# Performance work log

Hardware: AMD Instinct MI355X
Metric: run time of the kernel (lower is better)

## Reference

```python
import jax, jax.numpy as jnp
import numpy as np

DIM = 1024
NUM_HEAD = 16
DIM_HEAD = DIM // NUM_HEAD
MAX_SEQ_LEN = 4096
RMS_EPS = 1.1920928955078125e-07  # torch nn.RMSNorm default eps = finfo(fp32).eps
LIN_EPS = 1e-6
PAD_VAL = 1.0
THETA = 10000.0


def rmsnorm(x, g):
    return x * jax.lax.rsqrt(jnp.mean(x * x, axis=-1, keepdims=True) + RMS_EPS) * g


def setup_inputs() -> dict:
    key = jax.random.key(0)
    ks = jax.random.split(key, 20)
    B, L, C, D = 4, 2048, 256, DIM
    s = 1.0 / np.sqrt(D)
    inp = {
        "x": jax.random.normal(ks[0], (B, L, D), jnp.float32),
        "context": jax.random.normal(ks[1], (B, C, D), jnp.float32),
        "attn_mask": jax.random.randint(ks[2], (B, L, L), 0, 2).astype(bool),
        "start_pos": jax.random.randint(ks[3], (B,), 0, MAX_SEQ_LEN - L).astype(jnp.int64),
        "Wqkv": jax.random.normal(ks[4], (D, 3 * D), jnp.float32) * s,
        "bqkv": jax.random.normal(ks[5], (3 * D,), jnp.float32) * 0.01,
        "g_q": jnp.ones((D,), jnp.float32),
        "g_k": jnp.ones((D,), jnp.float32),
        "cWqkv": jax.random.normal(ks[6], (D, 3 * D), jnp.float32) * s,
        "cbqkv": jax.random.normal(ks[7], (3 * D,), jnp.float32) * 0.01,
        "cg_q": jnp.ones((D,), jnp.float32),
        "cg_k": jnp.ones((D,), jnp.float32),
        "Wout": jax.random.normal(ks[8], (D, D), jnp.float32) * s,
        "bout": jax.random.normal(ks[9], (D,), jnp.float32) * 0.01,
        "g_out": jnp.ones((D,), jnp.float32),
        "cWout": jax.random.normal(ks[10], (D, D), jnp.float32) * s,
        "cbout": jax.random.normal(ks[11], (D,), jnp.float32) * 0.01,
        "cg_out": jnp.ones((D,), jnp.float32),
    }
    return inp


def _freqs(pos_indices):
    # pos_indices: (B, L) int
    inv = 1.0 / (THETA ** (jnp.arange(0, DIM_HEAD, 2, dtype=jnp.float32) / DIM_HEAD))  # (DH/2,)
    ang = pos_indices.astype(jnp.float32)[..., None] * inv  # (B, L, DH/2)
    return jnp.cos(ang), jnp.sin(ang)


def _apply_rope(t, cos, sin):
    # t: (B, H, L, DH); cos/sin: (B, L, DH/2) -> broadcast over head
    B, H, L, DH = t.shape
    tr = t.reshape(B, H, L, DH // 2, 2)
    t0, t1 = tr[..., 0], tr[..., 1]
    c = cos[:, None]  # (B,1,L,DH/2)
    s = sin[:, None]
    out = jnp.stack([t0 * c - t1 * s, t0 * s + t1 * c], axis=-1)
    return out.reshape(B, H, L, DH)


def _split_heads(t):
    B, L, D = t.shape
    return t.reshape(B, L, NUM_HEAD, DIM_HEAD).transpose(0, 2, 1, 3)


def _augment_mask(m, C):
    # m: (B, L, L) bool -> (B, L+C, L+C) bool
    B, L, _ = m.shape
    c_to_seq = jnp.broadcast_to(jnp.any(m, axis=1, keepdims=True), (B, C, L))
    seq_to_c = jnp.broadcast_to(jnp.any(m, axis=2, keepdims=True), (B, L, C))
    c_to_c = jnp.ones((B, C, C), bool)
    top = jnp.concatenate([m, seq_to_c], axis=2)
    bot = jnp.concatenate([c_to_seq, c_to_c], axis=2)
    return jnp.concatenate([top, bot], axis=1)


def reference(x, context, attn_mask, start_pos, Wqkv, bqkv, g_q, g_k,
              cWqkv, cbqkv, cg_q, cg_k, Wout, bout, g_out, cWout, cbout, cg_out):
    B, L, D = x.shape
    C = context.shape[1]

    q, k, v = jnp.split(x @ Wqkv + bqkv, 3, axis=-1)
    q = rmsnorm(q, g_q)
    k = rmsnorm(k, g_k)
    q, k, v = _split_heads(q), _split_heads(k), _split_heads(v)  # (B,H,L,DH)

    pos = start_pos[:, None] + jnp.arange(L, dtype=start_pos.dtype)[None]  # (B,L)
    cos, sin = _freqs(pos)
    q = _apply_rope(q, cos, sin)
    k = _apply_rope(k, cos, sin)

    cq, ck, cv = jnp.split(context @ cWqkv + cbqkv, 3, axis=-1)
    cq = rmsnorm(cq, cg_q)
    ck = rmsnorm(ck, cg_k)
    cq, ck, cv = _split_heads(cq), _split_heads(ck), _split_heads(cv)

    q = jnp.concatenate([q, cq], axis=2)  # (B,H,S,DH), S=L+C
    k = jnp.concatenate([k, ck], axis=2)
    v = jnp.concatenate([v, cv], axis=2)

    full_mask = _augment_mask(attn_mask, C)[:, None]  # (B,1,S,S)

    # linear attention: ReLU feature map + padded-value trick
    qf = jax.nn.relu(q)
    kf = jax.nn.relu(k)
    k_mask = full_mask[:, :, 0, :][..., None].astype(kf.dtype)  # (B,1,S,1)
    kf = kf * k_mask
    vpad = jnp.pad(v, ((0, 0), (0, 0), (0, 0), (0, 1)), constant_values=PAD_VAL)  # (B,H,S,DH+1)
    vk = jnp.einsum('bhse,bhsd->bhed', vpad, kf)        # (B,H,DH+1,DH)
    res = jnp.einsum('bhed,bhqd->bhqe', vk, qf)          # (B,H,S,DH+1)
    attn = res[..., :-1] / (res[..., -1:] + LIN_EPS)     # (B,H,S,DH)

    attn = attn.transpose(0, 2, 1, 3).reshape(B, L + C, D)
    x_out = rmsnorm(attn[:, :L] @ Wout + bout, g_out)
    c_out = rmsnorm(attn[:, L:] @ cWout + cbout, cg_out)
    return x_out, c_out
```

## Files before the change

### kernel.cpp

```cpp
#include <hip/hip_runtime.h>

typedef __bf16 bf16;
typedef __bf16 bf16x4 __attribute__((ext_vector_type(4)));
typedef __bf16 bf16x8 __attribute__((ext_vector_type(8)));
typedef float  floatx4 __attribute__((ext_vector_type(4)));

#define L_SEQ   2048
#define C_SEQ   256
#define S_SEQ   2304
#define NBATCH  4
#define NHEAD   16
#define DHEAD   64
#define DMODEL  1024
#define RMS_EPS 1.1920928955078125e-07f
#define LIN_EPS 1e-6f

__device__ __forceinline__ void gload_lds16(const void* g, void* l) {
  __builtin_amdgcn_global_load_lds(
      (const __attribute__((address_space(1))) void*)g,
      (__attribute__((address_space(3))) void*)l, 16, 0, 0);
}

__device__ __forceinline__ void transpose_job(
    const float* __restrict__ src, bf16* __restrict__ dst,
    int R, int C, int tb, bf16 (*tile)[33]) {
  int tilesx = C >> 5;
  int c0 = (tb % tilesx) * 32, r0 = (tb / tilesx) * 32;
  int tx = threadIdx.x & 31, ty = threadIdx.x >> 5;
  for (int i = ty; i < 32; i += 8)
    tile[i][tx] = (bf16)src[(size_t)(r0 + i) * C + c0 + tx];
  __syncthreads();
  for (int i = ty; i < 32; i += 8)
    dst[(size_t)(c0 + i) * R + r0 + tx] = tile[tx][i];
}

__device__ __forceinline__ void convert_job(
    const float* __restrict__ src, bf16* __restrict__ dst, int tb) {
  size_t i = ((size_t)tb * 256 + threadIdx.x) * 8;
  floatx4 a = *(const floatx4*)(src + i);
  floatx4 b = *(const floatx4*)(src + i + 4);
  bf16x8 o;
#pragma unroll
  for (int j = 0; j < 4; j++) { o[j] = (bf16)a[j]; o[4 + j] = (bf16)b[j]; }
  *(bf16x8*)(dst + i) = o;
}

__global__ __launch_bounds__(256) void prep(
    const float* __restrict__ Wqkv, const float* __restrict__ cWqkv,
    const float* __restrict__ Wout, const float* __restrict__ cWout,
    const float* __restrict__ x, const float* __restrict__ ctx,
    const int* __restrict__ mask, const int* __restrict__ spos,
    bf16* __restrict__ WqkvT, bf16* __restrict__ cWqkvT,
    bf16* __restrict__ WoutT, bf16* __restrict__ cWoutT,
    bf16* __restrict__ xbf, bf16* __restrict__ cbf,
    float* __restrict__ vkw, float* __restrict__ rope,
    int* __restrict__ anym) {
  __shared__ bf16 tile[32][33];
  __shared__ int sh;
  int b = blockIdx.x;
  if (b < 3072) { transpose_job(Wqkv, WqkvT, 1024, 3072, b, tile); return; }
  b -= 3072;
  if (b < 3072) { transpose_job(cWqkv, cWqkvT, 1024, 3072, b, tile); return; }
  b -= 3072;
  if (b < 1024) { transpose_job(Wout, WoutT, 1024, 1024, b, tile); return; }
  b -= 1024;
  if (b < 1024) { transpose_job(cWout, cWoutT, 1024, 1024, b, tile); return; }
  b -= 1024;
  if (b < 4096) { convert_job(x, xbf, b); return; }
  b -= 4096;
  if (b < 512) { convert_job(ctx, cbf, b); return; }
  b -= 512;
  if (b < 260) {
    int i = b * 1024 + threadIdx.x * 4;
    *(floatx4*)(vkw + i) = floatx4{0.f, 0.f, 0.f, 0.f};
    return;
  }
  b -= 260;
  if (b < 2048) {
    int t = threadIdx.x;
    int tok = b * 4 + (t >> 6);
    int bb = tok >> 11, s = tok & 2047;
    int j = t & 63, fi = j >> 1;
    float ang = (float)(spos[bb] + s) * expf((float)fi * -0.28782313662425572f);
    rope[(size_t)tok * 64 + j] = (j & 1) ? sinf(ang) : cosf(ang);
    return;
  }
  b -= 2048;
  int a = 0;
  size_t base = (size_t)b * L_SEQ * L_SEQ;
  for (int j = threadIdx.x; j < L_SEQ; j += 256) a |= mask[base + j];
  if (threadIdx.x == 0) sh = 0;
  __syncthreads();
  if (a) atomicOr(&sh, 1);
  __syncthreads();
  if (threadIdx.x == 0) anym[b] = sh;
}

template <bool SCATTER>
__global__ __launch_bounds__(256) void gemm_bias(
    const bf16* __restrict__ A1, const bf16* __restrict__ A2,
    const bf16* __restrict__ B1t, const bf16* __restrict__ B2t,
    const float* __restrict__ bias1, const float* __restrict__ bias2,
    bf16* __restrict__ C1, bf16* __restrict__ C2,
    bf16* __restrict__ qs, bf16* __restrict__ ks, bf16* __restrict__ vs,
    int N, int K, int ybound,
    int rpb1, int soff1, int rpb2, int soff2) {
  __shared__ bf16 As[2][4096];
  __shared__ bf16 Bs[2][4096];

  int nwg = gridDim.x * gridDim.y;
  int wg = blockIdx.y * gridDim.x + blockIdx.x;
  int cpx = nwg >> 3;
  wg = (wg & 7) * cpx + (wg >> 3);
  int bx = wg % gridDim.x, by = wg / gridDim.x;
  int n0 = bx * 128;
  const bf16 *Ap, *Bt;
  const float* bias;
  bf16* Cp;
  int m0, rpb, soff;
  if (by < ybound) {
    Ap = A1; Bt = B1t; bias = bias1; Cp = C1;
    m0 = by * 128; rpb = rpb1; soff = soff1;
  } else {
    Ap = A2; Bt = B2t; bias = bias2; Cp = C2;
    m0 = (by - ybound) * 128; rpb = rpb2; soff = soff2;
  }

  int t = threadIdx.x, lane = t & 63, w = t >> 6;
  int wm = (w & 1) * 64, wn = (w >> 1) * 64;
  int l16 = lane & 15, l4 = lane >> 4;

  int crow = w * 32 + (lane >> 2);
  int scol = ((((lane & 3) - ((lane >> 3) & 3)) & 3)) << 3;
  const bf16* Ab = Ap + (size_t)(m0 + crow) * K + scol;
  const bf16* Bb = Bt + (size_t)(n0 + crow) * K + scol;

  auto stage = [&](int buf, int kb) {
#pragma unroll
    for (int j = 0; j < 2; j++) {
      gload_lds16(Ab + (size_t)(j * 16) * K + kb, (char*)As[buf] + (w * 2 + j) * 1024);
      gload_lds16(Bb + (size_t)(j * 16) * K + kb, (char*)Bs[buf] + (w * 2 + j) * 1024);
    }
  };

  int co = ((l4 + ((l16 >> 1) & 3)) & 3) << 3;
  int rba = (wm + l16) * 32 + co;
  int rbb = (wn + l16) * 32 + co;

  floatx4 acc[4][4] = {};
  stage(0, 0);
  __syncthreads();
  int NTt = K >> 5;
  for (int tt = 0; tt < NTt; ++tt) {
    int p = tt & 1;
    if (tt + 1 < NTt) stage(p ^ 1, (tt + 1) << 5);
    bf16x8 bfr[4];
#pragma unroll
    for (int nt = 0; nt < 4; nt++) bfr[nt] = *(const bf16x8*)&Bs[p][rbb + nt * 512];
    __builtin_amdgcn_s_setprio(1);
#pragma unroll
    for (int mt = 0; mt < 4; mt++) {
      bf16x8 a = *(const bf16x8*)&As[p][rba + mt * 512];
#pragma unroll
      for (int nt = 0; nt < 4; nt++)
        acc[mt][nt] = __builtin_amdgcn_mfma_f32_16x16x32_bf16(a, bfr[nt], acc[mt][nt], 0, 0, 0);
    }
    __builtin_amdgcn_s_setprio(0);
    __syncthreads();
  }

#pragma unroll
  for (int mt = 0; mt < 4; mt++)
#pragma unroll
    for (int nt = 0; nt < 4; nt++) {
      int col = n0 + wn + nt * 16 + l16;
      float bval = bias[col];
      if constexpr (SCATTER) {
        int which = col >> 10;
        int h = (col >> 6) & 15;
        int dh = col & 63;
        int rmask = (1 << rpb) - 1;
        if (which == 2) {
          int rw0 = m0 + wm + mt * 16 + l4 * 4;
          int b = rw0 >> rpb;
          int s = soff + (rw0 & rmask);
          bf16x4 o;
#pragma unroll
          for (int r = 0; r < 4; r++) o[r] = (bf16)(acc[mt][nt][r] + bval);
          *(bf16x4*)(vs + ((size_t)(b * NHEAD + h) * DHEAD + dh) * S_SEQ + s) = o;
        } else {
          bf16* dst = which == 0 ? qs : ks;
#pragma unroll
          for (int r = 0; r < 4; r++) {
            int rw = m0 + wm + mt * 16 + l4 * 4 + r;
            int b = rw >> rpb;
            int s = soff + (rw & rmask);
            dst[((size_t)(b * NHEAD + h) * S_SEQ + s) * DHEAD + dh] =
                (bf16)(acc[mt][nt][r] + bval);
          }
        }
      } else {
#pragma unroll
        for (int r = 0; r < 4; r++) {
          int rw = m0 + wm + mt * 16 + l4 * 4 + r;
          Cp[(size_t)rw * N + col] = (bf16)(acc[mt][nt][r] + bval);
        }
      }
    }
}

__global__ __launch_bounds__(256) void qkv_post(
    bf16* __restrict__ qs, bf16* __restrict__ ks,
    const int* __restrict__ mask, const float* __restrict__ rope,
    const int* __restrict__ anym,
    const float* __restrict__ g_q, const float* __restrict__ g_k,
    const float* __restrict__ cg_q, const float* __restrict__ cg_k) {
  int g = blockIdx.x, t = threadIdx.x;
  bool is_ctx = g >= NBATCH * L_SEQ;
  int b, s;
  const float *gq, *gk;
  float mval;
  if (!is_ctx) {
    b = g >> 11;
    int l = g & 2047;
    s = l;
    mval = mask[(size_t)b * L_SEQ * L_SEQ + l] ? 1.f : 0.f;
    gq = g_q; gk = g_k;
  } else {
    int gg = g - NBATCH * L_SEQ;
    b = gg >> 8;
    s = L_SEQ + (gg & 255);
    mval = anym[b] ? 1.f : 0.f;
    gq = cg_q; gk = cg_k;
  }
  int d0 = t * 4;
  int h = t >> 4, dh = (t & 15) * 4;
  size_t base = ((size_t)(b * NHEAD + h) * S_SEQ + s) * DHEAD + dh;
  bf16x4 q4 = *(const bf16x4*)(qs + base);
  bf16x4 k4 = *(const bf16x4*)(ks + base);
  float qv[4], kv[4], pq = 0.f, pk = 0.f;
#pragma unroll
  for (int i = 0; i < 4; i++) {
    qv[i] = (float)q4[i]; kv[i] = (float)k4[i];
    pq += qv[i] * qv[i];  pk += kv[i] * kv[i];
  }
  int lane = t & 63, w = t >> 6;
  for (int off = 32; off > 0; off >>= 1) {
    pq += __shfl_down(pq, off, 64);
    pk += __shfl_down(pk, off, 64);
  }
  __shared__ float red[8];
  if (lane == 0) { red[w] = pq; red[4 + w] = pk; }
  __syncthreads();
  float sq = red[0] + red[1] + red[2] + red[3];
  float sk = red[4] + red[5] + red[6] + red[7];
  float scq = rsqrtf(sq * (1.f / DMODEL) + RMS_EPS);
  float sck = rsqrtf(sk * (1.f / DMODEL) + RMS_EPS);
#pragma unroll
  for (int i = 0; i < 4; i++) {
    qv[i] *= scq * gq[d0 + i];
    kv[i] *= sck * gk[d0 + i];
  }
  if (!is_ctx) {
    floatx4 tb4 = *(const floatx4*)&rope[((size_t)(b << 11 | s)) * 64 + dh];
#pragma unroll
    for (int pr = 0; pr < 2; pr++) {
      float cc = tb4[2 * pr], ss = tb4[2 * pr + 1];
      float t0 = qv[2 * pr], t1 = qv[2 * pr + 1];
      qv[2 * pr]     = t0 * cc - t1 * ss;
      qv[2 * pr + 1] = t0 * ss + t1 * cc;
      t0 = kv[2 * pr]; t1 = kv[2 * pr + 1];
      kv[2 * pr]     = t0 * cc - t1 * ss;
      kv[2 * pr + 1] = t0 * ss + t1 * cc;
    }
  }
  bf16x4 qo, ko;
#pragma unroll
  for (int i = 0; i < 4; i++) {
    qo[i] = (bf16)fmaxf(qv[i], 0.f);
    ko[i] = (bf16)(fmaxf(kv[i], 0.f) * mval);
  }
  *(bf16x4*)(qs + base) = qo;
  *(bf16x4*)(ks + base) = ko;
}

#define VK_CH   12
#define VK_SPAN (S_SEQ / VK_CH)
__global__ __launch_bounds__(256) void vk_mfma(
    const bf16* __restrict__ vT, const bf16* __restrict__ kf,
    float* __restrict__ vk) {
  __shared__ bf16 Vs[2][64][40];
  __shared__ bf16 Ks[2][64][40];
  int bh = blockIdx.x / VK_CH, chunk = blockIdx.x % VK_CH;
  int t = threadIdx.x, lane = t & 63, w = t >> 6;
  int l16 = lane & 15, l4 = lane >> 4;
  const bf16* vp = vT + (size_t)bh * DHEAD * S_SEQ;
  const bf16* kp = kf + (size_t)bh * S_SEQ * DHEAD;
  int s_begin = chunk * VK_SPAN;
  int ve = t >> 2, vso = (t & 3) * 8;
  int ks_s = t & 31, kd0 = (t >> 5) * 8;
  floatx4 acc[4] = {};
  float dsum[8] = {};
  bf16x8 vv = *(const bf16x8*)(vp + (size_t)ve * S_SEQ + s_begin + vso);
  bf16x8 kv = *(const bf16x8*)(kp + (size_t)(s_begin + ks_s) * DHEAD + kd0);
  for (int st = 0; st < VK_SPAN; st += 32) {
    int cur = (st >> 5) & 1;
    *(bf16x8*)&Vs[cur][ve][vso] = vv;
#pragma unroll
    for (int j = 0; j < 8; j++) {
      Ks[cur][kd0 + j][ks_s] = kv[j];
      dsum[j] += (float)kv[j];
    }
    if (st + 32 < VK_SPAN) {
      int s0 = s_begin + st + 32;
      vv = *(const bf16x8*)(vp + (size_t)ve * S_SEQ + s0 + vso);
      kv = *(const bf16x8*)(kp + (size_t)(s0 + ks_s) * DHEAD + kd0);
    }
    __syncthreads();
    bf16x8 af = *(const bf16x8*)&Vs[cur][w * 16 + l16][l4 * 8];
#pragma unroll
    for (int nt = 0; nt < 4; nt++) {
      bf16x8 bfr = *(const bf16x8*)&Ks[cur][nt * 16 + l16][l4 * 8];
      acc[nt] = __builtin_amdgcn_mfma_f32_16x16x32_bf16(af, bfr, acc[nt], 0, 0, 0);
    }
  }
  float* vkbh = vk + (size_t)bh * 65 * 64;
#pragma unroll
  for (int nt = 0; nt < 4; nt++)
#pragma unroll
    for (int r = 0; r < 4; r++)
      atomicAdd(&vkbh[(w * 16 + l4 * 4 + r) * 64 + nt * 16 + l16], acc[nt][r]);
#pragma unroll
  for (int j = 0; j < 8; j++)
#pragma unroll
    for (int off = 16; off > 0; off >>= 1)
      dsum[j] += __shfl_down(dsum[j], off, 32);
  if ((lane & 31) == 0)
#pragma unroll
    for (int j = 0; j < 8; j++)
      atomicAdd(&vkbh[64 * 64 + kd0 + j], dsum[j]);
}

__global__ __launch_bounds__(256) void res_attn(
    const bf16* __restrict__ qf, const float* __restrict__ vk,
    bf16* __restrict__ attn_x, bf16* __restrict__ attn_c) {
  __shared__ bf16 Bs[80][72];
  __shared__ float sden[256];
  int bh = blockIdx.x / 9, mblk = blockIdx.x % 9;
  int b = bh >> 4, h = bh & 15;
  int t = threadIdx.x, lane = t & 63, w = t >> 6;
  const float* vkp = vk + (size_t)bh * 65 * 64;
  for (int i = t; i < 80 * 64; i += 256) {
    int e = i >> 6, d = i & 63;
    Bs[e][d] = (bf16)(e < 65 ? vkp[i] : 0.f);
  }
  __syncthreads();
  int l16 = lane & 15, l4 = lane >> 4;
  const bf16* qbase = qf + (size_t)bh * S_SEQ * DHEAD;
  int q0w = mblk * 256 + w * 64;

  floatx4 acc[4][5] = {};
  bf16x8 af[4][2], bfr[5][2];
#pragma unroll
  for (int mt = 0; mt < 4; mt++) {
    int q = q0w + mt * 16 + l16;
    af[mt][0] = *(const bf16x8*)(qbase + (size_t)q * 64 + l4 * 8);
    af[mt][1] = *(const bf16x8*)(qbase + (size_t)q * 64 + 32 + l4 * 8);
  }
#pragma unroll
  for (int nt = 0; nt < 5; nt++) {
    bfr[nt][0] = *(const bf16x8*)&Bs[nt * 16 + l16][l4 * 8];
    bfr[nt][1] = *(const bf16x8*)&Bs[nt * 16 + l16][32 + l4 * 8];
  }
#pragma unroll
  for (int mt = 0; mt < 4; mt++)
#pragma unroll
    for (int nt = 0; nt < 5; nt++) {
      acc[mt][nt] = __builtin_amdgcn_mfma_f32_16x16x32_bf16(af[mt][0], bfr[nt][0], acc[mt][nt], 0, 0, 0);
      acc[mt][nt] = __builtin_amdgcn_mfma_f32_16x16x32_bf16(af[mt][1], bfr[nt][1], acc[mt][nt], 0, 0, 0);
    }
  if (l16 == 0) {
#pragma unroll
    for (int mt = 0; mt < 4; mt++)
#pragma unroll
      for (int r = 0; r < 4; r++)
        sden[w * 64 + mt * 16 + l4 * 4 + r] = acc[mt][4][r];
  }
  __syncthreads();
#pragma unroll
  for (int mt = 0; mt < 4; mt++)
#pragma unroll
    for (int r = 0; r < 4; r++) {
      float den = sden[w * 64 + mt * 16 + l4 * 4 + r] + LIN_EPS;
      float rden = 1.f / den;
      int q = q0w + mt * 16 + l4 * 4 + r;
#pragma unroll
      for (int nt = 0; nt < 4; nt++) {
        int dcol = nt * 16 + l16;
        float a = acc[mt][nt][r] * rden;
        if (q < L_SEQ)
          attn_x[((size_t)b * L_SEQ + q) * DMODEL + h * DHEAD + dcol] = (bf16)a;
        else
          attn_c[((size_t)b * C_SEQ + (q - L_SEQ)) * DMODEL + h * DHEAD + dcol] = (bf16)a;
      }
    }
}

__global__ __launch_bounds__(256) void final_norm(
    const bf16* __restrict__ y_x, const bf16* __restrict__ y_c,
    const float* __restrict__ g_out, const float* __restrict__ cg_out,
    float* __restrict__ out) {
  int g = blockIdx.x, t = threadIdx.x;
  const bf16* src;
  const float* gv;
  if (g < NBATCH * L_SEQ) {
    src = y_x + (size_t)g * DMODEL; gv = g_out;
  } else {
    int gg = g - NBATCH * L_SEQ;
    src = y_c + (size_t)gg * DMODEL; gv = cg_out;
  }
  float* dst = out + (size_t)g * DMODEL;
  int d0 = t * 4;
  bf16x4 y4 = *(const bf16x4*)(src + d0);
  float yv[4], p = 0.f;
#pragma unroll
  for (int i = 0; i < 4; i++) { yv[i] = (float)y4[i]; p += yv[i] * yv[i]; }
  int lane = t & 63, w = t >> 6;
  for (int off = 32; off > 0; off >>= 1) p += __shfl_down(p, off, 64);
  __shared__ float red[4];
  if (lane == 0) red[w] = p;
  __syncthreads();
  float ssum = red[0] + red[1] + red[2] + red[3];
  float sc = rsqrtf(ssum * (1.f / DMODEL) + RMS_EPS);
  floatx4 o;
#pragma unroll
  for (int i = 0; i < 4; i++) o[i] = yv[i] * sc * gv[d0 + i];
  *(floatx4*)(dst + d0) = o;
}

extern "C" void kernel_launch(void* const* d_in, const int* in_sizes, int n_in,
                              void* d_out, int out_size, void* d_ws, size_t ws_size,
                              hipStream_t stream) {
  const float* x      = (const float*)d_in[0];
  const float* ctx    = (const float*)d_in[1];
  const int*   mask   = (const int*)d_in[2];
  const int*   spos   = (const int*)d_in[3];
  const float* Wqkv   = (const float*)d_in[4];
  const float* bqkv   = (const float*)d_in[5];
  const float* g_q    = (const float*)d_in[6];
  const float* g_k    = (const float*)d_in[7];
  const float* cWqkv  = (const float*)d_in[8];
  const float* cbqkv  = (const float*)d_in[9];
  const float* cg_q   = (const float*)d_in[10];
  const float* cg_k   = (const float*)d_in[11];
  const float* Wout   = (const float*)d_in[12];
  const float* bout   = (const float*)d_in[13];
  const float* g_out  = (const float*)d_in[14];
  const float* cWout  = (const float*)d_in[15];
  const float* cbout  = (const float*)d_in[16];
  const float* cg_out = (const float*)d_in[17];

  char* wsp = (char*)d_ws;
  size_t off = 0;
  auto alloc = [&](size_t bytes) -> void* {
    void* p = wsp + off;
    off += (bytes + 255) & ~(size_t)255;
    return p;
  };
  bf16* WqkvT  = (bf16*)alloc((size_t)3072 * 1024 * 2);
  bf16* cWqkvT = (bf16*)alloc((size_t)3072 * 1024 * 2);
  bf16* WoutT  = (bf16*)alloc((size_t)1024 * 1024 * 2);
  bf16* cWoutT = (bf16*)alloc((size_t)1024 * 1024 * 2);
  bf16* xbf    = (bf16*)alloc((size_t)NBATCH * L_SEQ * DMODEL * 2);
  bf16* cbf    = (bf16*)alloc((size_t)NBATCH * C_SEQ * DMODEL * 2);
  const size_t SLAB = (size_t)NBATCH * NHEAD * S_SEQ * DHEAD;
  bf16* qfs    = (bf16*)alloc(SLAB * 2);
  bf16* kfs    = (bf16*)alloc(SLAB * 2);
  bf16* vfs    = (bf16*)alloc(SLAB * 2);
  float* vkw   = (float*)alloc((size_t)64 * 65 * 64 * 4);
  float* rope  = (float*)alloc((size_t)NBATCH * L_SEQ * 64 * 4);
  int* anym    = (int*)alloc(256);
  bf16* attn_x = kfs;
  bf16* attn_c = kfs + (size_t)NBATCH * L_SEQ * DMODEL;
  bf16* y_x    = vfs;
  bf16* y_c    = vfs + (size_t)NBATCH * L_SEQ * DMODEL;

  prep<<<15112, 256, 0, stream>>>(Wqkv, cWqkv, Wout, cWout, x, ctx, mask, spos,
                                  WqkvT, cWqkvT, WoutT, cWoutT, xbf, cbf,
                                  vkw, rope, anym);

  gemm_bias<true><<<dim3(24, 72), 256, 0, stream>>>(
      xbf, cbf, WqkvT, cWqkvT, bqkv, cbqkv, nullptr, nullptr,
      qfs, kfs, vfs, 3072, 1024, 64, 11, 0, 8, L_SEQ);

  qkv_post<<<NBATCH * (L_SEQ + C_SEQ), 256, 0, stream>>>(
      qfs, kfs, mask, rope, anym, g_q, g_k, cg_q, cg_k);

  vk_mfma<<<64 * VK_CH, 256, 0, stream>>>(vfs, kfs, vkw);

  res_attn<<<576, 256, 0, stream>>>(qfs, vkw, attn_x, attn_c);

  gemm_bias<false><<<dim3(8, 72), 256, 0, stream>>>(
      attn_x, attn_c, WoutT, cWoutT, bout, cbout, y_x, y_c,
      nullptr, nullptr, nullptr, 1024, 1024, 64, 0, 0, 0, 0);

  final_norm<<<NBATCH * (L_SEQ + C_SEQ), 256, 0, stream>>>(
      y_x, y_c, g_out, cg_out, (float*)d_out);
}
```

Before: 360.2 us.

## Add 256x256-tile 8-wave QKV GEMM with interleaved staged loads

Replaces the 128x128-tile QKV projection GEMM with a new kernel using 256x256 tiles, 512 threads (8 waves) and a 64-wide K step. Global-to-LDS loads are split into quarter stages spread across the MFMA phases, using a two-deep prefetch with explicit vmcnt waits and an XOR-swizzled LDS layout. The goal is more operand reuse per tile and better overlap of loads with matrix math. In exchange it uses 128 KB of LDS per block and many more accumulator registers, and the grid shrinks to 432 blocks, which may limit occupancy.

```diff
diff --git a/kernel.cpp b/kernel.cpp
--- a/kernel.cpp
+++ b/kernel.cpp
@@ -96,6 +96,142 @@
   if (threadIdx.x == 0) anym[b] = sh;
 }
 
+__global__ __launch_bounds__(512, 2) void gemm_qkv8(
+    const bf16* __restrict__ A1, const bf16* __restrict__ A2,
+    const bf16* __restrict__ B1t, const bf16* __restrict__ B2t,
+    const float* __restrict__ bias1, const float* __restrict__ bias2,
+    bf16* __restrict__ qs, bf16* __restrict__ ks, bf16* __restrict__ vs,
+    int K, int ybound, int rpb1, int soff1, int rpb2, int soff2) {
+  __shared__ bf16 As[2][256 * 64];
+  __shared__ bf16 Bs[2][256 * 64];
+
+  int nwg = gridDim.x * gridDim.y;
+  int wg = blockIdx.y * gridDim.x + blockIdx.x;
+  int cpx = nwg >> 3;
+  wg = (wg & 7) * cpx + (wg >> 3);
+  int bx = wg % gridDim.x, by = wg / gridDim.x;
+  int n0 = bx * 256;
+  const bf16 *Ap, *Bt;
+  const float* bias;
+  int m0, rpb, soff;
+  if (by < ybound) {
+    Ap = A1; Bt = B1t; bias = bias1; m0 = by * 256; rpb = rpb1; soff = soff1;
+  } else {
+    Ap = A2; Bt = B2t; bias = bias2; m0 = (by - ybound) * 256; rpb = rpb2; soff = soff2;
+  }
+
+  int t = threadIdx.x, lane = t & 63, w = t >> 6;
+  int wr = w >> 2, wc = w & 3;
+  int l16 = lane & 15, l4 = lane >> 4;
+
+  int lr = lane >> 3;
+  int lcol = ((lane & 7) ^ lr) << 3;
+  const bf16* Ag = Ap + (size_t)(m0 + lr) * K + lcol;
+  const bf16* Bg = Bt + (size_t)(n0 + lr) * K + lcol;
+
+  int cB0 = w * 2;
+  int cB1 = 16 + w * 2;
+  int cAX = ((w & 4) << 2) + (w & 3) * 2;
+  int cAY = 8 + cAX;
+
+  auto stg = [&](const bf16* G, bf16* Ldst, int c0, int kb) {
+#pragma unroll
+    for (int j = 0; j < 2; j++) {
+      int c = c0 + j;
+      gload_lds16(G + (size_t)(c * 8) * K + kb, (char*)Ldst + c * 1024);
+    }
+  };
+  auto ldf = [&](const bf16* S, int row, int ks) {
+    return *(const bf16x8*)&S[row * 64 + ((((ks << 2) + l4) ^ (l16 & 7)) << 3)];
+  };
+
+  floatx4 acc[8][4] = {};
+  int NT = K >> 6;
+  stg(Bg, Bs[0], cB0, 0);  stg(Bg, Bs[0], cB1, 0);
+  stg(Ag, As[0], cAX, 0);  stg(Ag, As[0], cAY, 0);
+  if (NT > 1) {
+    stg(Bg, Bs[1], cB0, 64); stg(Bg, Bs[1], cB1, 64);
+    stg(Ag, As[1], cAX, 64);
+  }
+  asm volatile("s_waitcnt vmcnt(6)" ::: "memory");
+  __builtin_amdgcn_s_barrier();
+
+  int pb = 0;
+  bf16x8 bfr[4][2];
+  for (int tt = 0; tt < NT; ++tt) {
+    int kb = tt << 6;
+    const bf16* Asp = As[pb];
+    const bf16* Bsp = Bs[pb];
+#pragma unroll
+    for (int p = 0; p < 4; ++p) {
+      if (p == 0) {
+#pragma unroll
+        for (int nt = 0; nt < 4; nt++) {
+          bfr[nt][0] = ldf(Bsp, wc * 64 + nt * 16 + l16, 0);
+          bfr[nt][1] = ldf(Bsp, wc * 64 + nt * 16 + l16, 1);
+        }
+      }
+      int ar = wr * 128 + p * 32 + l16;
+      bf16x8 a00 = ldf(Asp, ar, 0);
+      bf16x8 a01 = ldf(Asp, ar, 1);
+      bf16x8 a10 = ldf(Asp, ar + 16, 0);
+      bf16x8 a11 = ldf(Asp, ar + 16, 1);
+      if (p == 0)      { if (tt + 1 < NT) stg(Ag, As[pb ^ 1], cAY, kb + 64); }
+      else if (p == 1) { if (tt + 2 < NT) stg(Bg, Bs[pb], cB0, kb + 128); }
+      else if (p == 2) { if (tt + 2 < NT) stg(Bg, Bs[pb], cB1, kb + 128); }
+      else             { if (tt + 2 < NT) stg(Ag, As[pb], cAX, kb + 128); }
+      __builtin_amdgcn_s_barrier();
+      __builtin_amdgcn_s_setprio(1);
+      int mt = p * 2;
+#pragma unroll
+      for (int nt = 0; nt < 4; nt++) {
+        acc[mt][nt]     = __builtin_amdgcn_mfma_f32_16x16x32_bf16(a00, bfr[nt][0], acc[mt][nt], 0, 0, 0);
+        acc[mt][nt]     = __builtin_amdgcn_mfma_f32_16x16x32_bf16(a01, bfr[nt][1], acc[mt][nt], 0, 0, 0);
+        acc[mt + 1][nt] = __builtin_amdgcn_mfma_f32_16x16x32_bf16(a10, bfr[nt][0], acc[mt + 1][nt], 0, 0, 0);
+        acc[mt + 1][nt] = __builtin_amdgcn_mfma_f32_16x16x32_bf16(a11, bfr[nt][1], acc[mt + 1][nt], 0, 0, 0);
+      }
+      __builtin_amdgcn_s_setprio(0);
+      if (p == 3) {
+        if (tt + 2 < NT) asm volatile("s_waitcnt vmcnt(6)" ::: "memory");
+        else             asm volatile("s_waitcnt vmcnt(0)" ::: "memory");
+      }
+      __builtin_amdgcn_s_barrier();
+    }
+    pb ^= 1;
+  }
+
+#pragma unroll
+  for (int mt = 0; mt < 8; mt++)
+#pragma unroll
+    for (int nt = 0; nt < 4; nt++) {
+      int col = n0 + wc * 64 + nt * 16 + l16;
+      float bval = bias[col];
+      int which = col >> 10;
+      int h = (col >> 6) & 15;
+      int dh = col & 63;
+      int rmask = (1 << rpb) - 1;
+      if (which == 2) {
+        int rw0 = m0 + wr * 128 + mt * 16 + l4 * 4;
+        int b = rw0 >> rpb;
+        int s = soff + (rw0 & rmask);
+        bf16x4 o;
+#pragma unroll
+        for (int r = 0; r < 4; r++) o[r] = (bf16)(acc[mt][nt][r] + bval);
+        *(bf16x4*)(vs + ((size_t)(b * NHEAD + h) * DHEAD + dh) * S_SEQ + s) = o;
+      } else {
+        bf16* dst = which == 0 ? qs : ks;
+#pragma unroll
+        for (int r = 0; r < 4; r++) {
+          int rw = m0 + wr * 128 + mt * 16 + l4 * 4 + r;
+          int b = rw >> rpb;
+          int s = soff + (rw & rmask);
+          dst[((size_t)(b * NHEAD + h) * S_SEQ + s) * DHEAD + dh] =
+              (bf16)(acc[mt][nt][r] + bval);
+        }
+      }
+    }
+}
+
 template <bool SCATTER>
 __global__ __launch_bounds__(256) void gemm_bias(
     const bf16* __restrict__ A1, const bf16* __restrict__ A2,
@@ -107,7 +243,6 @@
     int rpb1, int soff1, int rpb2, int soff2) {
   __shared__ bf16 As[2][4096];
   __shared__ bf16 Bs[2][4096];
-
   int nwg = gridDim.x * gridDim.y;
   int wg = blockIdx.y * gridDim.x + blockIdx.x;
   int cpx = nwg >> 3;
@@ -125,16 +260,13 @@
     Ap = A2; Bt = B2t; bias = bias2; Cp = C2;
     m0 = (by - ybound) * 128; rpb = rpb2; soff = soff2;
   }
-
   int t = threadIdx.x, lane = t & 63, w = t >> 6;
   int wm = (w & 1) * 64, wn = (w >> 1) * 64;
   int l16 = lane & 15, l4 = lane >> 4;
-
   int crow = w * 32 + (lane >> 2);
   int scol = ((((lane & 3) - ((lane >> 3) & 3)) & 3)) << 3;
   const bf16* Ab = Ap + (size_t)(m0 + crow) * K + scol;
   const bf16* Bb = Bt + (size_t)(n0 + crow) * K + scol;
-
   auto stage = [&](int buf, int kb) {
 #pragma unroll
     for (int j = 0; j < 2; j++) {
@@ -142,11 +274,9 @@
       gload_lds16(Bb + (size_t)(j * 16) * K + kb, (char*)Bs[buf] + (w * 2 + j) * 1024);
     }
   };
-
   int co = ((l4 + ((l16 >> 1) & 3)) & 3) << 3;
   int rba = (wm + l16) * 32 + co;
   int rbb = (wn + l16) * 32 + co;
-
   floatx4 acc[4][4] = {};
   stage(0, 0);
   __syncthreads();
@@ -168,7 +298,6 @@
     __builtin_amdgcn_s_setprio(0);
     __syncthreads();
   }
-
 #pragma unroll
   for (int mt = 0; mt < 4; mt++)
 #pragma unroll
@@ -489,9 +618,9 @@
                                   WqkvT, cWqkvT, WoutT, cWoutT, xbf, cbf,
                                   vkw, rope, anym);
 
-  gemm_bias<true><<<dim3(24, 72), 256, 0, stream>>>(
-      xbf, cbf, WqkvT, cWqkvT, bqkv, cbqkv, nullptr, nullptr,
-      qfs, kfs, vfs, 3072, 1024, 64, 11, 0, 8, L_SEQ);
+  gemm_qkv8<<<dim3(12, 36), 512, 0, stream>>>(
+      xbf, cbf, WqkvT, cWqkvT, bqkv, cbqkv,
+      qfs, kfs, vfs, 1024, 32, 11, 0, 8, L_SEQ);
 
   qkv_post<<<NBATCH * (L_SEQ + C_SEQ), 256, 0, stream>>>(
       qfs, kfs, mask, rope, anym, g_q, g_k, cg_q, cg_k);
```

Measured after the change: 347.7 us. -3.4%, faster.
